# Performance work log

Measured on AMD Instinct MI355X. Metric: run time of the kernel, lower is better.

Reference implementation:

```python
import jax, jax.numpy as jnp
import numpy as np

VOCAB, EMBED, HIDDEN, LAYERS, CLASSES = 32000, 256, 256, 2, 2


def setup_inputs() -> dict:
    key = jax.random.key(0)
    ks = jax.random.split(key, 8)
    B, T = 64, 4096
    IN = EMBED + HIDDEN  # 512 (same for both layers since embed==hidden)
    tokens = jax.random.randint(ks[0], (B, T), 0, VOCAB)
    emb = jax.random.normal(ks[1], (VOCAB, EMBED), dtype=jnp.float32) * 0.05
    Wr = jax.random.normal(ks[2], (LAYERS, IN, HIDDEN), dtype=jnp.float32) * 0.05
    Wz = jax.random.normal(ks[3], (LAYERS, IN, HIDDEN), dtype=jnp.float32) * 0.05
    Wh = jax.random.normal(ks[4], (LAYERS, IN, HIDDEN), dtype=jnp.float32) * 0.05
    br = jnp.zeros((LAYERS, HIDDEN), dtype=jnp.float32)
    bz = jnp.full((LAYERS, HIDDEN), -2.0, dtype=jnp.float32)  # nn.init.constant_(bias_z, -2.0)
    bh = jnp.zeros((LAYERS, HIDDEN), dtype=jnp.float32)
    Wfc = jax.random.normal(ks[5], (HIDDEN, CLASSES), dtype=jnp.float32) * 0.05
    bfc = jnp.zeros((CLASSES,), dtype=jnp.float32)
    return dict(tokens=tokens, emb=emb, Wr=Wr, br=br, Wz=Wz, bz=bz, Wh=Wh, bh=bh, Wfc=Wfc, bfc=bfc)


def reference(tokens, emb, Wr, br, Wz, bz, Wh, bh, Wfc, bfc):
    B, T = tokens.shape
    x_seq = emb[tokens]                       # [B,T,E]
    xs = jnp.swapaxes(x_seq, 0, 1)            # [T,B,E] for scan over time
    h0 = jnp.zeros((LAYERS, B, HIDDEN), dtype=emb.dtype)

    def step(hs, xt):
        x = xt
        new_hs = []
        for i in range(LAYERS):
            h = hs[i]
            comb = jnp.concatenate([x, h], axis=1)          # [B, E+H]
            r = jax.nn.sigmoid(comb @ Wr[i] + br[i])
            z = jax.nn.sigmoid(comb @ Wz[i] + bz[i])
            comb_r = jnp.concatenate([x, r * h], axis=1)
            h_tilde = jnp.tanh(comb_r @ Wh[i] + bh[i])
            h = (1.0 - z) * h + z * h_tilde
            new_hs.append(h)
            x = h
        return jnp.stack(new_hs), None

    hs_final, _ = jax.lax.scan(step, h0, xs)
    # classification head on last timestep of last layer
    return hs_final[-1] @ Wfc + bfc             # [B, num_classes]
```

## Files before the change

### kernel.cpp

```cpp
#include <hip/hip_runtime.h>
#include <hip/hip_bf16.h>
#include <hip/hip_fp16.h>
#include <stdint.h>

typedef _Float16 h2_t  __attribute__((ext_vector_type(2)));
typedef _Float16 f16x8 __attribute__((ext_vector_type(8)));
typedef float    f32x4 __attribute__((ext_vector_type(4)));

#define TSEQ 4096
#define HID  256
#define IN2  512
#define NB   64
#define CH   256
#define NCH  16

__device__ __forceinline__ h2_t bc_h2(uint32_t v){ return __builtin_bit_cast(h2_t, v); }
__device__ __forceinline__ uint32_t pk2(float a, float b){
    h2_t p; p[0] = (_Float16)a; p[1] = (_Float16)b;
    return __builtin_bit_cast(uint32_t, p);
}

__device__ __forceinline__ float quad_reduce(float x){
    float t;
    t = __builtin_bit_cast(float, __builtin_amdgcn_mov_dpp(__builtin_bit_cast(int, x), 0xB1, 0xF, 0xF, true));
    x += t;
    t = __builtin_bit_cast(float, __builtin_amdgcn_mov_dpp(__builtin_bit_cast(int, x), 0x4E, 0xF, 0xF, true));
    x += t;
    return x;
}

__device__ __forceinline__ float sigm_(float x){
    return __builtin_amdgcn_rcpf(1.f + __expf(-x));
}
__device__ __forceinline__ float tanh_(float x){
    return 1.f - 2.f*__builtin_amdgcn_rcpf(1.f + __expf(2.f*x));
}

__device__ __forceinline__ void sync_lds(){
    asm volatile("s_waitcnt lgkmcnt(0)\n\ts_barrier" ::: "memory");
}

__global__ void prep_kernel(const float* __restrict__ Wr, const float* __restrict__ Wz,
                            const float* __restrict__ Wh, const float* __restrict__ emb,
                            const float* __restrict__ br, const float* __restrict__ bz,
                            const float* __restrict__ bh,
                            uint32_t* __restrict__ wpack, __half* __restrict__ wxt,
                            __half* __restrict__ embf16, float* __restrict__ biasv)
{
    const long long S0 = 2LL*3*128*256;
    const long long S1 = 2LL*768*256;
    const long long S2 = 32000LL*256;
    const long long S3 = 2LL*768;
    for (long long idx = (long long)blockIdx.x*256 + threadIdx.x; idx < S0+S1+S2+S3;
         idx += (long long)gridDim.x*256) {
        if (idx < S0) {
            int n   = (int)(idx & 255);
            int kk  = (int)((idx >> 8) & 127);
            int t   = (int)(idx >> 15);
            int g = t % 3, L = t / 3;
            const float* Wsrc = (g==0?Wr:(g==1?Wz:Wh)) + (size_t)L*IN2*HID;
            h2_t p;
            p[0] = (_Float16)Wsrc[(256 + kk)*HID + n];
            p[1] = (_Float16)Wsrc[(256 + 128 + kk)*HID + n];
            wpack[idx] = __builtin_bit_cast(uint32_t, p);
        } else if (idx < S0+S1) {
            int i  = (int)(idx - S0);
            int k  = i & 255;
            int i2 = i >> 8;
            int o  = i2 % 768, L = i2 / 768;
            int g  = o >> 8,   n = o & 255;
            const float* Wsrc = (g==0?Wr:(g==1?Wz:Wh)) + (size_t)L*IN2*HID;
            int ksrc = (L==1) ? ((k & 1) ? 128 + (k >> 1) : (k >> 1)) : k;
            wxt[i] = __float2half(Wsrc[ksrc*HID + n]);
        } else if (idx < S0+S1+S2) {
            int i = (int)(idx - S0 - S1);
            embf16[i] = __float2half(emb[i]);
        } else {
            int i = (int)(idx - S0 - S1 - S2);
            int o = i % 768, L = i / 768;
            int g = o >> 8,  n = o & 255;
            const float* bsrc = (g==0?br:(g==1?bz:bh));
            biasv[i] = bsrc[L*HID + n];
        }
    }
}

__global__ __launch_bounds__(256) void gemm_proj(
    const int* __restrict__ tokens, const __half* __restrict__ embf16,
    const __half* __restrict__ h0chunk, const __half* __restrict__ wxt,
    const float* __restrict__ biasv,
    __half* __restrict__ proj0, __half* __restrict__ proj1, int c0, int c1)
{
    const int Lz = blockIdx.z;
    const int c  = Lz ? c1 : c0;
    if (c < 0 || c >= NCH) return;
    __half* proj = Lz ? proj1 : proj0;

    __shared__ uint4 Ald[128*17];
    __shared__ uint4 Bld[64*17];
    const int tid = threadIdx.x;
    const int mt = blockIdx.x, nt = blockIdx.y;
    const int w = tid >> 6, l = tid & 63, lr = l & 15, lk = l >> 4;
    f32x4 acc[2][4] = {};

#pragma unroll 1
    for (int kh = 0; kh < 2; ++kh) {
        if (kh) __syncthreads();
#pragma unroll
        for (int it = 0; it < 8; ++it) {
            int idx = it*256 + tid;
            int row = idx >> 4, u4 = idx & 15;
            int grow = mt*128 + row;
            const __half* src;
            if (Lz == 0) {
                int b = grow >> 8, tl = grow & (CH-1);
                int tok = tokens[(size_t)b*TSEQ + c*CH + tl];
                src = embf16 + (size_t)tok*HID;
            } else {
                src = h0chunk + (size_t)grow*HID;
            }
            Ald[row*17 + u4] = ((const uint4*)(src + kh*128))[u4];
        }
#pragma unroll
        for (int it = 0; it < 4; ++it) {
            int idx = it*256 + tid;
            int col = idx >> 4, u4 = idx & 15;
            const __half* src = wxt + ((size_t)(Lz*768 + nt*64 + col))*HID + kh*128;
            Bld[col*17 + u4] = ((const uint4*)src)[u4];
        }
        __syncthreads();
        const _Float16* A = (const _Float16*)Ald;
        const _Float16* B = (const _Float16*)Bld;
#pragma unroll
        for (int kb = 0; kb < 4; ++kb) {
            int k0 = kb*32;
            f16x8 af[2], bf[4];
#pragma unroll
            for (int fm = 0; fm < 2; ++fm) {
                int row = w*32 + fm*16 + lr;
                af[fm] = *(const f16x8*)(A + row*136 + k0 + lk*8);
            }
#pragma unroll
            for (int fn = 0; fn < 4; ++fn) {
                int col = fn*16 + lr;
                bf[fn] = *(const f16x8*)(B + col*136 + k0 + lk*8);
            }
#pragma unroll
            for (int fm = 0; fm < 2; ++fm)
#pragma unroll
                for (int fn = 0; fn < 4; ++fn)
                    acc[fm][fn] = __builtin_amdgcn_mfma_f32_16x16x32_f16(af[fm], bf[fn], acc[fm][fn], 0,0,0);
        }
    }
#pragma unroll
    for (int fm = 0; fm < 2; ++fm)
#pragma unroll
        for (int fn = 0; fn < 4; ++fn)
#pragma unroll
            for (int q = 0; q < 4; ++q) {
                int row = mt*128 + w*32 + fm*16 + lk*4 + q;
                int col = nt*64 + fn*16 + lr;
                float v = acc[fm][fn][q] + biasv[Lz*768 + col];
                int nb2 = col & 127, g = col >> 8, hf2 = (col >> 7) & 1;
                proj[(size_t)row*1024 + nb2*8 + g*2 + hf2] = __float2half(v);
            }
}

__global__ __launch_bounds__(512)
__attribute__((amdgpu_waves_per_eu(2, 2)))
void rec_fused(
    const uint32_t* __restrict__ wpack,
    const __half* __restrict__ proj0, const __half* __restrict__ proj1,
    __half* __restrict__ h0chunk, float* __restrict__ hstate,
    const float* __restrict__ Wfc, const float* __restrict__ bfc,
    float* __restrict__ out, int c0, int c1)
{
    __shared__ __align__(16) uint32_t s_h[128];
    __shared__ __align__(16) uint32_t s_rh[128];
    __shared__ float s_head[256];

    const int L = blockIdx.x >> 6;
    const int b = blockIdx.x & 63;
    const int c = L ? c1 : c0;
    if (c < 0 || c >= NCH) return;

    const int tid = threadIdx.x;
    const int k4  = tid & 3;
    const int nb  = tid >> 2;
    const bool wlead = (k4 == 0);

    uint32_t wr_[2][32], wz_[2][32], wh_[2][32];
    {
        const uint32_t* wb = wpack + (size_t)(L*3*128)*256;
#pragma unroll
        for (int u = 0; u < 8; ++u)
#pragma unroll
            for (int j = 0; j < 4; ++j) {
                int i  = u*4 + j;
                int kk = k4*32 + (((u + k4) & 7)*4 + j);
                wr_[0][i] = wb[(      kk)*256 + nb      ];
                wr_[1][i] = wb[(      kk)*256 + nb + 128];
                wz_[0][i] = wb[(128 + kk)*256 + nb      ];
                wz_[1][i] = wb[(128 + kk)*256 + nb + 128];
                wh_[0][i] = wb[(256 + kk)*256 + nb      ];
                wh_[1][i] = wb[(256 + kk)*256 + nb + 128];
            }
    }
#pragma unroll
    for (int i = 0; i < 32; ++i) {
        asm volatile("" : "+v"(wr_[0][i]), "+v"(wr_[1][i]), "+v"(wz_[0][i]),
                          "+v"(wz_[1][i]), "+v"(wh_[0][i]), "+v"(wh_[1][i]));
    }

    float h0f, h1f;
    if (c == 0) { h0f = 0.f; h1f = 0.f; }
    else {
        h0f = hstate[(size_t)(L*NB + b)*HID + nb];
        h1f = hstate[(size_t)(L*NB + b)*HID + nb + 128];
    }
    if (wlead) s_h[nb] = pk2(h0f, h1f);
    __syncthreads();

    const uint4* prow = (const uint4*)((L ? proj1 : proj0) + (size_t)b*CH*1024);
    const uint4* hq4  = ((const uint4*)s_h)  + k4*8;
    const uint4* rq4  = ((const uint4*)s_rh) + k4*8;

    uint4 pj = prow[nb];

#pragma unroll 1
    for (int tl = 0; tl < CH; ++tl) {
        int tn = (tl + 1 < CH) ? tl + 1 : tl;
        uint4 pjN = prow[(size_t)tn*128 + nb];

        float ar0=0.f, ar1=0.f, az0=0.f, az1=0.f;
#pragma unroll
        for (int u = 0; u < 8; ++u) {
            uint4 hv = hq4[(u + k4) & 7];
            int i = u*4;
            ar0 = __builtin_amdgcn_fdot2(bc_h2(wr_[0][i  ]), bc_h2(hv.x), ar0, false);
            ar1 = __builtin_amdgcn_fdot2(bc_h2(wr_[1][i  ]), bc_h2(hv.x), ar1, false);
            az0 = __builtin_amdgcn_fdot2(bc_h2(wz_[0][i  ]), bc_h2(hv.x), az0, false);
            az1 = __builtin_amdgcn_fdot2(bc_h2(wz_[1][i  ]), bc_h2(hv.x), az1, false);
            ar0 = __builtin_amdgcn_fdot2(bc_h2(wr_[0][i+1]), bc_h2(hv.y), ar0, false);
            ar1 = __builtin_amdgcn_fdot2(bc_h2(wr_[1][i+1]), bc_h2(hv.y), ar1, false);
            az0 = __builtin_amdgcn_fdot2(bc_h2(wz_[0][i+1]), bc_h2(hv.y), az0, false);
            az1 = __builtin_amdgcn_fdot2(bc_h2(wz_[1][i+1]), bc_h2(hv.y), az1, false);
            ar0 = __builtin_amdgcn_fdot2(bc_h2(wr_[0][i+2]), bc_h2(hv.z), ar0, false);
            ar1 = __builtin_amdgcn_fdot2(bc_h2(wr_[1][i+2]), bc_h2(hv.z), ar1, false);
            az0 = __builtin_amdgcn_fdot2(bc_h2(wz_[0][i+2]), bc_h2(hv.z), az0, false);
            az1 = __builtin_amdgcn_fdot2(bc_h2(wz_[1][i+2]), bc_h2(hv.z), az1, false);
            ar0 = __builtin_amdgcn_fdot2(bc_h2(wr_[0][i+3]), bc_h2(hv.w), ar0, false);
            ar1 = __builtin_amdgcn_fdot2(bc_h2(wr_[1][i+3]), bc_h2(hv.w), ar1, false);
            az0 = __builtin_amdgcn_fdot2(bc_h2(wz_[0][i+3]), bc_h2(hv.w), az0, false);
            az1 = __builtin_amdgcn_fdot2(bc_h2(wz_[1][i+3]), bc_h2(hv.w), az1, false);
        }
        ar0 = quad_reduce(ar0); ar1 = quad_reduce(ar1);
        az0 = quad_reduce(az0); az1 = quad_reduce(az1);

        h2_t pjr = bc_h2(pj.x), pjz = bc_h2(pj.y);
        float r0 = sigm_(ar0 + (float)pjr[0]);
        float r1 = sigm_(ar1 + (float)pjr[1]);
        float z0 = sigm_(az0 + (float)pjz[0]);
        float z1 = sigm_(az1 + (float)pjz[1]);
        if (wlead) s_rh[nb] = pk2(r0*h0f, r1*h1f);
        sync_lds();

        float ah0a=0.f, ah0b=0.f, ah1a=0.f, ah1b=0.f;
#pragma unroll
        for (int u = 0; u < 8; ++u) {
            uint4 rv = rq4[(u + k4) & 7];
            int i = u*4;
            ah0a = __builtin_amdgcn_fdot2(bc_h2(wh_[0][i  ]), bc_h2(rv.x), ah0a, false);
            ah1a = __builtin_amdgcn_fdot2(bc_h2(wh_[1][i  ]), bc_h2(rv.x), ah1a, false);
            ah0b = __builtin_amdgcn_fdot2(bc_h2(wh_[0][i+1]), bc_h2(rv.y), ah0b, false);
            ah1b = __builtin_amdgcn_fdot2(bc_h2(wh_[1][i+1]), bc_h2(rv.y), ah1b, false);
            ah0a = __builtin_amdgcn_fdot2(bc_h2(wh_[0][i+2]), bc_h2(rv.z), ah0a, false);
            ah1a = __builtin_amdgcn_fdot2(bc_h2(wh_[1][i+2]), bc_h2(rv.z), ah1a, false);
            ah0b = __builtin_amdgcn_fdot2(bc_h2(wh_[0][i+3]), bc_h2(rv.w), ah0b, false);
            ah1b = __builtin_amdgcn_fdot2(bc_h2(wh_[1][i+3]), bc_h2(rv.w), ah1b, false);
        }
        float ah0 = quad_reduce(ah0a + ah0b);
        float ah1 = quad_reduce(ah1a + ah1b);

        h2_t pjh = bc_h2(pj.z);
        float t0 = tanh_(ah0 + (float)pjh[0]);
        float t1 = tanh_(ah1 + (float)pjh[1]);
        h0f += z0*(t0 - h0f);
        h1f += z1*(t1 - h1f);
        if (wlead) {
            uint32_t w2 = pk2(h0f, h1f);
            s_h[nb] = w2;
            if (L == 0)
                ((uint32_t*)h0chunk)[((size_t)b*CH + tl)*128 + nb] = w2;
        }
        pj = pjN;
        sync_lds();
    }

    if (wlead) {
        hstate[(size_t)(L*NB + b)*HID + nb]       = h0f;
        hstate[(size_t)(L*NB + b)*HID + nb + 128] = h1f;
    }

    if (L == 1 && c == NCH-1) {
        if (wlead) { s_head[nb] = h0f; s_head[nb+128] = h1f; }
        __syncthreads();
        if (tid < 64) {
            float p0 = 0.f, p1 = 0.f;
#pragma unroll
            for (int m = 0; m < 4; ++m) {
                float hv2 = s_head[tid + 64*m];
                p0 += hv2 * Wfc[(tid+64*m)*2+0];
                p1 += hv2 * Wfc[(tid+64*m)*2+1];
            }
#pragma unroll
            for (int d = 1; d < 64; d <<= 1) { p0 += __shfl_xor(p0, d); p1 += __shfl_xor(p1, d); }
            if (tid == 0) { out[b*2+0] = p0 + bfc[0]; out[b*2+1] = p1 + bfc[1]; }
        }
    }
}

extern "C" void kernel_launch(void* const* d_in, const int* in_sizes, int n_in,
                              void* d_out, int out_size, void* d_ws, size_t ws_size,
                              hipStream_t stream) {
    const int*   tokens = (const int*)  d_in[0];
    const float* emb    = (const float*)d_in[1];
    const float* Wr     = (const float*)d_in[2];
    const float* br     = (const float*)d_in[3];
    const float* Wz     = (const float*)d_in[4];
    const float* bz     = (const float*)d_in[5];
    const float* Wh     = (const float*)d_in[6];
    const float* bh     = (const float*)d_in[7];
    const float* Wfc    = (const float*)d_in[8];
    const float* bfc    = (const float*)d_in[9];
    float* out = (float*)d_out;

    char* ws = (char*)d_ws;
    uint32_t* wpack  = (uint32_t*)(ws + 0);
    __half*   wxt    = (__half*)(ws + (1u<<20));
    __half*   embf16 = (__half*)(ws + (2u<<20));
    __half*   proj0  = (__half*)(ws + 18874368u);
    __half*   proj1  = (__half*)(ws + 52428800u);
    __half*   h0chunk= (__half*)(ws + 85983232u);
    float*    hstate = (float*)(ws + 94371840u);
    float*    biasv  = (float*)(ws + 94502912u);

    prep_kernel<<<2048, 256, 0, stream>>>(Wr, Wz, Wh, emb, br, bz, bh, wpack, wxt, embf16, biasv);

    dim3 ggrid(128, 12, 2);
    for (int c = 0; c <= NCH; ++c) {
        int cc0 = (c < NCH) ? c : -1;
        int cc1 = c - 1;
        gemm_proj<<<ggrid, 256, 0, stream>>>(tokens, embf16, h0chunk, wxt, biasv, proj0, proj1, cc0, cc1);
        rec_fused<<<128, 512, 0, stream>>>(wpack, proj0, proj1, h0chunk, hstate, Wfc, bfc, out, cc0, cc1);
    }
}
```

Measured before the change: 7.011 ms.

## Fuse projection GEMM and recurrence into one launch with double-buffered pipelining

The separate projection GEMM and recurrence kernels are merged into a single launch per step. The first 128 blocks run the recurrence for chunk `step` (layer 0) and `step-2` (layer 1), while the remaining blocks compute projections for upcoming chunks into double-buffered proj and h0 buffers. This lets the small, latency-bound recurrence overlap with the GEMM instead of running serially. It also removes the fp16 embedding conversion pass by converting fp32 embeddings on the fly, compacts the proj layout to 768 halves per row, and uses 128x128 GEMM tiles. The cost is larger LDS per block, which may reduce occupancy for the recurrence blocks, and one extra pipeline step.

```diff
diff --git a/kernel.cpp b/kernel.cpp
--- a/kernel.cpp
+++ b/kernel.cpp
@@ -19,7 +19,6 @@
     h2_t p; p[0] = (_Float16)a; p[1] = (_Float16)b;
     return __builtin_bit_cast(uint32_t, p);
 }
-
 __device__ __forceinline__ float quad_reduce(float x){
     float t;
     t = __builtin_bit_cast(float, __builtin_amdgcn_mov_dpp(__builtin_bit_cast(int, x), 0xB1, 0xF, 0xF, true));
@@ -28,35 +27,34 @@
     x += t;
     return x;
 }
-
 __device__ __forceinline__ float sigm_(float x){
     return __builtin_amdgcn_rcpf(1.f + __expf(-x));
 }
 __device__ __forceinline__ float tanh_(float x){
     return 1.f - 2.f*__builtin_amdgcn_rcpf(1.f + __expf(2.f*x));
 }
-
 __device__ __forceinline__ void sync_lds(){
     asm volatile("s_waitcnt lgkmcnt(0)\n\ts_barrier" ::: "memory");
 }
+__device__ __forceinline__ f32x4 mfma16(f16x8 a, f16x8 b, f32x4 c){
+    return __builtin_amdgcn_mfma_f32_16x16x32_f16(a, b, c, 0, 0, 0);
+}
 
 __global__ void prep_kernel(const float* __restrict__ Wr, const float* __restrict__ Wz,
-                            const float* __restrict__ Wh, const float* __restrict__ emb,
+                            const float* __restrict__ Wh,
                             const float* __restrict__ br, const float* __restrict__ bz,
                             const float* __restrict__ bh,
                             uint32_t* __restrict__ wpack, __half* __restrict__ wxt,
-                            __half* __restrict__ embf16, float* __restrict__ biasv)
+                            float* __restrict__ biasv)
 {
-    const long long S0 = 2LL*3*128*256;
-    const long long S1 = 2LL*768*256;
-    const long long S2 = 32000LL*256;
-    const long long S3 = 2LL*768;
-    for (long long idx = (long long)blockIdx.x*256 + threadIdx.x; idx < S0+S1+S2+S3;
-         idx += (long long)gridDim.x*256) {
+    const int S0 = 196608;
+    const int S1 = 393216;
+    const int S3 = 1536;
+    for (int idx = blockIdx.x*256 + threadIdx.x; idx < S0+S1+S3; idx += gridDim.x*256) {
         if (idx < S0) {
-            int n   = (int)(idx & 255);
-            int kk  = (int)((idx >> 8) & 127);
-            int t   = (int)(idx >> 15);
+            int n  = idx & 255;
+            int kk = (idx >> 8) & 127;
+            int t  = idx >> 15;
             int g = t % 3, L = t / 3;
             const float* Wsrc = (g==0?Wr:(g==1?Wz:Wh)) + (size_t)L*IN2*HID;
             h2_t p;
@@ -64,19 +62,16 @@
             p[1] = (_Float16)Wsrc[(256 + 128 + kk)*HID + n];
             wpack[idx] = __builtin_bit_cast(uint32_t, p);
         } else if (idx < S0+S1) {
-            int i  = (int)(idx - S0);
+            int i  = idx - S0;
             int k  = i & 255;
             int i2 = i >> 8;
             int o  = i2 % 768, L = i2 / 768;
             int g  = o >> 8,   n = o & 255;
             const float* Wsrc = (g==0?Wr:(g==1?Wz:Wh)) + (size_t)L*IN2*HID;
             int ksrc = (L==1) ? ((k & 1) ? 128 + (k >> 1) : (k >> 1)) : k;
-            wxt[i] = __float2half(Wsrc[ksrc*HID + n]);
-        } else if (idx < S0+S1+S2) {
-            int i = (int)(idx - S0 - S1);
-            embf16[i] = __float2half(emb[i]);
+            wxt[i] = __float2half(Wsrc[(size_t)ksrc*HID + n]);
         } else {
-            int i = (int)(idx - S0 - S1 - S2);
+            int i = idx - S0 - S1;
             int o = i % 768, L = i / 768;
             int g = o >> 8,  n = o & 255;
             const float* bsrc = (g==0?br:(g==1?bz:bh));
@@ -85,238 +80,258 @@
     }
 }
 
-__global__ __launch_bounds__(256) void gemm_proj(
-    const int* __restrict__ tokens, const __half* __restrict__ embf16,
-    const __half* __restrict__ h0chunk, const __half* __restrict__ wxt,
-    const float* __restrict__ biasv,
-    __half* __restrict__ proj0, __half* __restrict__ proj1, int c0, int c1)
-{
-    const int Lz = blockIdx.z;
-    const int c  = Lz ? c1 : c0;
-    if (c < 0 || c >= NCH) return;
-    __half* proj = Lz ? proj1 : proj0;
-
-    __shared__ uint4 Ald[128*17];
-    __shared__ uint4 Bld[64*17];
-    const int tid = threadIdx.x;
-    const int mt = blockIdx.x, nt = blockIdx.y;
-    const int w = tid >> 6, l = tid & 63, lr = l & 15, lk = l >> 4;
-    f32x4 acc[2][4] = {};
-
-#pragma unroll 1
-    for (int kh = 0; kh < 2; ++kh) {
-        if (kh) __syncthreads();
-#pragma unroll
-        for (int it = 0; it < 8; ++it) {
-            int idx = it*256 + tid;
-            int row = idx >> 4, u4 = idx & 15;
-            int grow = mt*128 + row;
-            const __half* src;
-            if (Lz == 0) {
-                int b = grow >> 8, tl = grow & (CH-1);
-                int tok = tokens[(size_t)b*TSEQ + c*CH + tl];
-                src = embf16 + (size_t)tok*HID;
-            } else {
-                src = h0chunk + (size_t)grow*HID;
-            }
-            Ald[row*17 + u4] = ((const uint4*)(src + kh*128))[u4];
-        }
-#pragma unroll
-        for (int it = 0; it < 4; ++it) {
-            int idx = it*256 + tid;
-            int col = idx >> 4, u4 = idx & 15;
-            const __half* src = wxt + ((size_t)(Lz*768 + nt*64 + col))*HID + kh*128;
-            Bld[col*17 + u4] = ((const uint4*)src)[u4];
-        }
-        __syncthreads();
-        const _Float16* A = (const _Float16*)Ald;
-        const _Float16* B = (const _Float16*)Bld;
-#pragma unroll
-        for (int kb = 0; kb < 4; ++kb) {
-            int k0 = kb*32;
-            f16x8 af[2], bf[4];
-#pragma unroll
-            for (int fm = 0; fm < 2; ++fm) {
-                int row = w*32 + fm*16 + lr;
-                af[fm] = *(const f16x8*)(A + row*136 + k0 + lk*8);
-            }
-#pragma unroll
-            for (int fn = 0; fn < 4; ++fn) {
-                int col = fn*16 + lr;
-                bf[fn] = *(const f16x8*)(B + col*136 + k0 + lk*8);
-            }
-#pragma unroll
-            for (int fm = 0; fm < 2; ++fm)
-#pragma unroll
-                for (int fn = 0; fn < 4; ++fn)
-                    acc[fm][fn] = __builtin_amdgcn_mfma_f32_16x16x32_f16(af[fm], bf[fn], acc[fm][fn], 0,0,0);
-        }
-    }
-#pragma unroll
-    for (int fm = 0; fm < 2; ++fm)
-#pragma unroll
-        for (int fn = 0; fn < 4; ++fn)
-#pragma unroll
-            for (int q = 0; q < 4; ++q) {
-                int row = mt*128 + w*32 + fm*16 + lk*4 + q;
-                int col = nt*64 + fn*16 + lr;
-                float v = acc[fm][fn][q] + biasv[Lz*768 + col];
-                int nb2 = col & 127, g = col >> 8, hf2 = (col >> 7) & 1;
-                proj[(size_t)row*1024 + nb2*8 + g*2 + hf2] = __float2half(v);
-            }
-}
-
 __global__ __launch_bounds__(512)
 __attribute__((amdgpu_waves_per_eu(2, 2)))
-void rec_fused(
-    const uint32_t* __restrict__ wpack,
-    const __half* __restrict__ proj0, const __half* __restrict__ proj1,
-    __half* __restrict__ h0chunk, float* __restrict__ hstate,
-    const float* __restrict__ Wfc, const float* __restrict__ bfc,
-    float* __restrict__ out, int c0, int c1)
+void fused_step(const int* __restrict__ tokens, const float* __restrict__ emb,
+                const uint32_t* __restrict__ wpack, const __half* __restrict__ wxt,
+                const float* __restrict__ biasv,
+                __half* __restrict__ proj0a, __half* __restrict__ proj0b,
+                __half* __restrict__ proj1a, __half* __restrict__ proj1b,
+                __half* __restrict__ h0a, __half* __restrict__ h0b,
+                float* __restrict__ hstate,
+                const float* __restrict__ Wfc, const float* __restrict__ bfc,
+                float* __restrict__ out, int step)
 {
     __shared__ __align__(16) uint32_t s_h[128];
     __shared__ __align__(16) uint32_t s_rh[128];
     __shared__ float s_head[256];
-
-    const int L = blockIdx.x >> 6;
-    const int b = blockIdx.x & 63;
-    const int c = L ? c1 : c0;
-    if (c < 0 || c >= NCH) return;
+    __shared__ uint4 Ald[128*17];
+    __shared__ uint4 Bld[128*17];
 
     const int tid = threadIdx.x;
-    const int k4  = tid & 3;
-    const int nb  = tid >> 2;
-    const bool wlead = (k4 == 0);
-
-    uint32_t wr_[2][32], wz_[2][32], wh_[2][32];
-    {
-        const uint32_t* wb = wpack + (size_t)(L*3*128)*256;
-#pragma unroll
-        for (int u = 0; u < 8; ++u)
-#pragma unroll
-            for (int j = 0; j < 4; ++j) {
-                int i  = u*4 + j;
-                int kk = k4*32 + (((u + k4) & 7)*4 + j);
-                wr_[0][i] = wb[(      kk)*256 + nb      ];
-                wr_[1][i] = wb[(      kk)*256 + nb + 128];
-                wz_[0][i] = wb[(128 + kk)*256 + nb      ];
-                wz_[1][i] = wb[(128 + kk)*256 + nb + 128];
-                wh_[0][i] = wb[(256 + kk)*256 + nb      ];
-                wh_[1][i] = wb[(256 + kk)*256 + nb + 128];
-            }
-    }
-#pragma unroll
-    for (int i = 0; i < 32; ++i) {
-        asm volatile("" : "+v"(wr_[0][i]), "+v"(wr_[1][i]), "+v"(wz_[0][i]),
-                          "+v"(wz_[1][i]), "+v"(wh_[0][i]), "+v"(wh_[1][i]));
-    }
-
-    float h0f, h1f;
-    if (c == 0) { h0f = 0.f; h1f = 0.f; }
-    else {
-        h0f = hstate[(size_t)(L*NB + b)*HID + nb];
-        h1f = hstate[(size_t)(L*NB + b)*HID + nb + 128];
-    }
-    if (wlead) s_h[nb] = pk2(h0f, h1f);
-    __syncthreads();
-
-    const uint4* prow = (const uint4*)((L ? proj1 : proj0) + (size_t)b*CH*1024);
-    const uint4* hq4  = ((const uint4*)s_h)  + k4*8;
-    const uint4* rq4  = ((const uint4*)s_rh) + k4*8;
-
-    uint4 pj = prow[nb];
+
+    if (blockIdx.x < 128) {
+        const int L = blockIdx.x >> 6;
+        const int b = blockIdx.x & 63;
+        const int c = L ? (step - 2) : step;
+        if (c < 0 || c >= NCH) return;
+        const uint32_t* projr = (const uint32_t*)(L ? ((step & 1) ? proj1b : proj1a)
+                                                    : ((step & 1) ? proj0b : proj0a));
+        uint32_t* h0w = (uint32_t*)((step & 1) ? h0b : h0a);
+
+        const int k4  = tid & 3;
+        const int nb  = tid >> 2;
+        const bool wlead = (k4 == 0);
+
+        uint32_t wr_[2][32], wz_[2][32], wh_[2][32];
+        {
+            const uint32_t* wb = wpack + (size_t)(L*3*128)*256;
+#pragma unroll
+            for (int u = 0; u < 8; ++u)
+#pragma unroll
+                for (int j = 0; j < 4; ++j) {
+                    int i  = u*4 + j;
+                    int kk = k4*32 + (((u + k4) & 7)*4 + j);
+                    wr_[0][i] = wb[(      kk)*256 + nb      ];
+                    wr_[1][i] = wb[(      kk)*256 + nb + 128];
+                    wz_[0][i] = wb[(128 + kk)*256 + nb      ];
+                    wz_[1][i] = wb[(128 + kk)*256 + nb + 128];
+                    wh_[0][i] = wb[(256 + kk)*256 + nb      ];
+                    wh_[1][i] = wb[(256 + kk)*256 + nb + 128];
+                }
+        }
+#pragma unroll
+        for (int i = 0; i < 32; ++i) {
+            asm volatile("" : "+v"(wr_[0][i]), "+v"(wr_[1][i]), "+v"(wz_[0][i]),
+                              "+v"(wz_[1][i]), "+v"(wh_[0][i]), "+v"(wh_[1][i]));
+        }
+
+        float h0f, h1f;
+        if (c == 0) { h0f = 0.f; h1f = 0.f; }
+        else {
+            h0f = hstate[(size_t)(L*NB + b)*HID + nb];
+            h1f = hstate[(size_t)(L*NB + b)*HID + nb + 128];
+        }
+        if (wlead) s_h[nb] = pk2(h0f, h1f);
+        __syncthreads();
+
+        const uint32_t* prow = projr + (size_t)b*CH*384;
+        const uint4* hq4  = ((const uint4*)s_h)  + k4*8;
+        const uint4* rq4  = ((const uint4*)s_rh) + k4*8;
+
+        uint2    pjrz = *(const uint2*)(prow + nb*2);
+        uint32_t pjh  = prow[256 + nb];
 
 #pragma unroll 1
-    for (int tl = 0; tl < CH; ++tl) {
-        int tn = (tl + 1 < CH) ? tl + 1 : tl;
-        uint4 pjN = prow[(size_t)tn*128 + nb];
-
-        float ar0=0.f, ar1=0.f, az0=0.f, az1=0.f;
-#pragma unroll
-        for (int u = 0; u < 8; ++u) {
-            uint4 hv = hq4[(u + k4) & 7];
-            int i = u*4;
-            ar0 = __builtin_amdgcn_fdot2(bc_h2(wr_[0][i  ]), bc_h2(hv.x), ar0, false);
-            ar1 = __builtin_amdgcn_fdot2(bc_h2(wr_[1][i  ]), bc_h2(hv.x), ar1, false);
-            az0 = __builtin_amdgcn_fdot2(bc_h2(wz_[0][i  ]), bc_h2(hv.x), az0, false);
-            az1 = __builtin_amdgcn_fdot2(bc_h2(wz_[1][i  ]), bc_h2(hv.x), az1, false);
-            ar0 = __builtin_amdgcn_fdot2(bc_h2(wr_[0][i+1]), bc_h2(hv.y), ar0, false);
-            ar1 = __builtin_amdgcn_fdot2(bc_h2(wr_[1][i+1]), bc_h2(hv.y), ar1, false);
-            az0 = __builtin_amdgcn_fdot2(bc_h2(wz_[0][i+1]), bc_h2(hv.y), az0, false);
-            az1 = __builtin_amdgcn_fdot2(bc_h2(wz_[1][i+1]), bc_h2(hv.y), az1, false);
-            ar0 = __builtin_amdgcn_fdot2(bc_h2(wr_[0][i+2]), bc_h2(hv.z), ar0, false);
-            ar1 = __builtin_amdgcn_fdot2(bc_h2(wr_[1][i+2]), bc_h2(hv.z), ar1, false);
-            az0 = __builtin_amdgcn_fdot2(bc_h2(wz_[0][i+2]), bc_h2(hv.z), az0, false);
-            az1 = __builtin_amdgcn_fdot2(bc_h2(wz_[1][i+2]), bc_h2(hv.z), az1, false);
-            ar0 = __builtin_amdgcn_fdot2(bc_h2(wr_[0][i+3]), bc_h2(hv.w), ar0, false);
-            ar1 = __builtin_amdgcn_fdot2(bc_h2(wr_[1][i+3]), bc_h2(hv.w), ar1, false);
-            az0 = __builtin_amdgcn_fdot2(bc_h2(wz_[0][i+3]), bc_h2(hv.w), az0, false);
-            az1 = __builtin_amdgcn_fdot2(bc_h2(wz_[1][i+3]), bc_h2(hv.w), az1, false);
-        }
-        ar0 = quad_reduce(ar0); ar1 = quad_reduce(ar1);
-        az0 = quad_reduce(az0); az1 = quad_reduce(az1);
-
-        h2_t pjr = bc_h2(pj.x), pjz = bc_h2(pj.y);
-        float r0 = sigm_(ar0 + (float)pjr[0]);
-        float r1 = sigm_(ar1 + (float)pjr[1]);
-        float z0 = sigm_(az0 + (float)pjz[0]);
-        float z1 = sigm_(az1 + (float)pjz[1]);
-        if (wlead) s_rh[nb] = pk2(r0*h0f, r1*h1f);
-        sync_lds();
-
-        float ah0a=0.f, ah0b=0.f, ah1a=0.f, ah1b=0.f;
-#pragma unroll
-        for (int u = 0; u < 8; ++u) {
-            uint4 rv = rq4[(u + k4) & 7];
-            int i = u*4;
-            ah0a = __builtin_amdgcn_fdot2(bc_h2(wh_[0][i  ]), bc_h2(rv.x), ah0a, false);
-            ah1a = __builtin_amdgcn_fdot2(bc_h2(wh_[1][i  ]), bc_h2(rv.x), ah1a, false);
-            ah0b = __builtin_amdgcn_fdot2(bc_h2(wh_[0][i+1]), bc_h2(rv.y), ah0b, false);
-            ah1b = __builtin_amdgcn_fdot2(bc_h2(wh_[1][i+1]), bc_h2(rv.y), ah1b, false);
-            ah0a = __builtin_amdgcn_fdot2(bc_h2(wh_[0][i+2]), bc_h2(rv.z), ah0a, false);
-            ah1a = __builtin_amdgcn_fdot2(bc_h2(wh_[1][i+2]), bc_h2(rv.z), ah1a, false);
-            ah0b = __builtin_amdgcn_fdot2(bc_h2(wh_[0][i+3]), bc_h2(rv.w), ah0b, false);
-            ah1b = __builtin_amdgcn_fdot2(bc_h2(wh_[1][i+3]), bc_h2(rv.w), ah1b, false);
-        }
-        float ah0 = quad_reduce(ah0a + ah0b);
-        float ah1 = quad_reduce(ah1a + ah1b);
-
-        h2_t pjh = bc_h2(pj.z);
-        float t0 = tanh_(ah0 + (float)pjh[0]);
-        float t1 = tanh_(ah1 + (float)pjh[1]);
-        h0f += z0*(t0 - h0f);
-        h1f += z1*(t1 - h1f);
+        for (int tl = 0; tl < CH; ++tl) {
+            int tn = (tl + 1 < CH) ? tl + 1 : tl;
+            const uint32_t* pn = prow + (size_t)tn*384;
+            uint2    pjrzN = *(const uint2*)(pn + nb*2);
+            uint32_t pjhN  = pn[256 + nb];
+
+            float ar0=0.f, ar1=0.f, az0=0.f, az1=0.f;
+#pragma unroll
+            for (int u = 0; u < 8; ++u) {
+                uint4 hv = hq4[(u + k4) & 7];
+                int i = u*4;
+                ar0 = __builtin_amdgcn_fdot2(bc_h2(wr_[0][i  ]), bc_h2(hv.x), ar0, false);
+                ar1 = __builtin_amdgcn_fdot2(bc_h2(wr_[1][i  ]), bc_h2(hv.x), ar1, false);
+                az0 = __builtin_amdgcn_fdot2(bc_h2(wz_[0][i  ]), bc_h2(hv.x), az0, false);
+                az1 = __builtin_amdgcn_fdot2(bc_h2(wz_[1][i  ]), bc_h2(hv.x), az1, false);
+                ar0 = __builtin_amdgcn_fdot2(bc_h2(wr_[0][i+1]), bc_h2(hv.y), ar0, false);
+                ar1 = __builtin_amdgcn_fdot2(bc_h2(wr_[1][i+1]), bc_h2(hv.y), ar1, false);
+                az0 = __builtin_amdgcn_fdot2(bc_h2(wz_[0][i+1]), bc_h2(hv.y), az0, false);
+                az1 = __builtin_amdgcn_fdot2(bc_h2(wz_[1][i+1]), bc_h2(hv.y), az1, false);
+                ar0 = __builtin_amdgcn_fdot2(bc_h2(wr_[0][i+2]), bc_h2(hv.z), ar0, false);
+                ar1 = __builtin_amdgcn_fdot2(bc_h2(wr_[1][i+2]), bc_h2(hv.z), ar1, false);
+                az0 = __builtin_amdgcn_fdot2(bc_h2(wz_[0][i+2]), bc_h2(hv.z), az0, false);
+                az1 = __builtin_amdgcn_fdot2(bc_h2(wz_[1][i+2]), bc_h2(hv.z), az1, false);
+                ar0 = __builtin_amdgcn_fdot2(bc_h2(wr_[0][i+3]), bc_h2(hv.w), ar0, false);
+                ar1 = __builtin_amdgcn_fdot2(bc_h2(wr_[1][i+3]), bc_h2(hv.w), ar1, false);
+                az0 = __builtin_amdgcn_fdot2(bc_h2(wz_[0][i+3]), bc_h2(hv.w), az0, false);
+                az1 = __builtin_amdgcn_fdot2(bc_h2(wz_[1][i+3]), bc_h2(hv.w), az1, false);
+            }
+            ar0 = quad_reduce(ar0); ar1 = quad_reduce(ar1);
+            az0 = quad_reduce(az0); az1 = quad_reduce(az1);
+
+            h2_t pjr = bc_h2(pjrz.x), pjz = bc_h2(pjrz.y);
+            float r0 = sigm_(ar0 + (float)pjr[0]);
+            float r1 = sigm_(ar1 + (float)pjr[1]);
+            float z0 = sigm_(az0 + (float)pjz[0]);
+            float z1 = sigm_(az1 + (float)pjz[1]);
+            if (wlead) s_rh[nb] = pk2(r0*h0f, r1*h1f);
+            sync_lds();
+
+            float ah0a=0.f, ah0b=0.f, ah1a=0.f, ah1b=0.f;
+#pragma unroll
+            for (int u = 0; u < 8; ++u) {
+                uint4 rv = rq4[(u + k4) & 7];
+                int i = u*4;
+                ah0a = __builtin_amdgcn_fdot2(bc_h2(wh_[0][i  ]), bc_h2(rv.x), ah0a, false);
+                ah1a = __builtin_amdgcn_fdot2(bc_h2(wh_[1][i  ]), bc_h2(rv.x), ah1a, false);
+                ah0b = __builtin_amdgcn_fdot2(bc_h2(wh_[0][i+1]), bc_h2(rv.y), ah0b, false);
+                ah1b = __builtin_amdgcn_fdot2(bc_h2(wh_[1][i+1]), bc_h2(rv.y), ah1b, false);
+                ah0a = __builtin_amdgcn_fdot2(bc_h2(wh_[0][i+2]), bc_h2(rv.z), ah0a, false);
+                ah1a = __builtin_amdgcn_fdot2(bc_h2(wh_[1][i+2]), bc_h2(rv.z), ah1a, false);
+                ah0b = __builtin_amdgcn_fdot2(bc_h2(wh_[0][i+3]), bc_h2(rv.w), ah0b, false);
+                ah1b = __builtin_amdgcn_fdot2(bc_h2(wh_[1][i+3]), bc_h2(rv.w), ah1b, false);
+            }
+            float ah0 = quad_reduce(ah0a + ah0b);
+            float ah1 = quad_reduce(ah1a + ah1b);
+
+            h2_t pjh2 = bc_h2(pjh);
+            float t0 = tanh_(ah0 + (float)pjh2[0]);
+            float t1 = tanh_(ah1 + (float)pjh2[1]);
+            h0f += z0*(t0 - h0f);
+            h1f += z1*(t1 - h1f);
+            if (wlead) {
+                uint32_t w2 = pk2(h0f, h1f);
+                s_h[nb] = w2;
+                if (L == 0)
+                    h0w[((size_t)b*CH + tl)*128 + nb] = w2;
+            }
+            pjrz = pjrzN; pjh = pjhN;
+            sync_lds();
+        }
+
         if (wlead) {
-            uint32_t w2 = pk2(h0f, h1f);
-            s_h[nb] = w2;
-            if (L == 0)
-                ((uint32_t*)h0chunk)[((size_t)b*CH + tl)*128 + nb] = w2;
-        }
-        pj = pjN;
-        sync_lds();
-    }
-
-    if (wlead) {
-        hstate[(size_t)(L*NB + b)*HID + nb]       = h0f;
-        hstate[(size_t)(L*NB + b)*HID + nb + 128] = h1f;
-    }
-
-    if (L == 1 && c == NCH-1) {
-        if (wlead) { s_head[nb] = h0f; s_head[nb+128] = h1f; }
-        __syncthreads();
-        if (tid < 64) {
-            float p0 = 0.f, p1 = 0.f;
-#pragma unroll
-            for (int m = 0; m < 4; ++m) {
-                float hv2 = s_head[tid + 64*m];
-                p0 += hv2 * Wfc[(tid+64*m)*2+0];
-                p1 += hv2 * Wfc[(tid+64*m)*2+1];
-            }
-#pragma unroll
-            for (int d = 1; d < 64; d <<= 1) { p0 += __shfl_xor(p0, d); p1 += __shfl_xor(p1, d); }
-            if (tid == 0) { out[b*2+0] = p0 + bfc[0]; out[b*2+1] = p1 + bfc[1]; }
-        }
+            hstate[(size_t)(L*NB + b)*HID + nb]       = h0f;
+            hstate[(size_t)(L*NB + b)*HID + nb + 128] = h1f;
+        }
+
+        if (L == 1 && c == NCH-1) {
+            if (wlead) { s_head[nb] = h0f; s_head[nb+128] = h1f; }
+            __syncthreads();
+            if (tid < 64) {
+                float p0 = 0.f, p1 = 0.f;
+#pragma unroll
+                for (int m = 0; m < 4; ++m) {
+                    float hv2 = s_head[tid + 64*m];
+                    p0 += hv2 * Wfc[(tid+64*m)*2+0];
+                    p1 += hv2 * Wfc[(tid+64*m)*2+1];
+                }
+#pragma unroll
+                for (int d = 1; d < 64; d <<= 1) { p0 += __shfl_xor(p0, d); p1 += __shfl_xor(p1, d); }
+                if (tid == 0) { out[b*2+0] = p0 + bfc[0]; out[b*2+1] = p1 + bfc[1]; }
+            }
+        }
+    } else {
+        int gb = blockIdx.x - 128;
+        const int Lz = (gb >= 768) ? 1 : 0;
+        gb -= Lz * 768;
+        const int mt = gb / 6, nt = gb % 6;
+        const int c = Lz ? (step - 1) : (step + 1);
+        if (c < 0 || c >= NCH) return;
+        __half* projw = Lz ? (((step + 1) & 1) ? proj1b : proj1a)
+                           : (((step + 1) & 1) ? proj0b : proj0a);
+        const __half* h0r = ((step - 1) & 1) ? h0b : h0a;
+
+        const int w  = tid >> 6;
+        const int wm = w >> 2, wn = w & 3;
+        const int l  = tid & 63, lr = l & 15, lk = l >> 4;
+        f32x4 acc[4][2] = {};
+
+#pragma unroll 1
+        for (int kh = 0; kh < 2; ++kh) {
+            if (kh) __syncthreads();
+            if (Lz == 0) {
+#pragma unroll
+                for (int it = 0; it < 4; ++it) {
+                    int idx = it*512 + tid;
+                    int row = idx >> 4, seg = idx & 15;
+                    int grow = mt*128 + row;
+                    int bb = grow >> 8, tl = grow & 255;
+                    int tok = tokens[(size_t)bb*TSEQ + c*CH + tl];
+                    const float* s = emb + (size_t)tok*HID + kh*128 + seg*8;
+                    float4 f0 = *(const float4*)s;
+                    float4 f1 = *(const float4*)(s + 4);
+                    uint4 v;
+                    v.x = __builtin_bit_cast(uint32_t, __builtin_amdgcn_cvt_pkrtz(f0.x, f0.y));
+                    v.y = __builtin_bit_cast(uint32_t, __builtin_amdgcn_cvt_pkrtz(f0.z, f0.w));
+                    v.z = __builtin_bit_cast(uint32_t, __builtin_amdgcn_cvt_pkrtz(f1.x, f1.y));
+                    v.w = __builtin_bit_cast(uint32_t, __builtin_amdgcn_cvt_pkrtz(f1.z, f1.w));
+                    Ald[row*17 + seg] = v;
+                }
+            } else {
+#pragma unroll
+                for (int it = 0; it < 4; ++it) {
+                    int idx = it*512 + tid;
+                    int row = idx >> 4, u4 = idx & 15;
+                    int grow = mt*128 + row;
+                    const __half* src = h0r + (size_t)grow*HID + kh*128;
+                    Ald[row*17 + u4] = ((const uint4*)src)[u4];
+                }
+            }
+#pragma unroll
+            for (int it = 0; it < 4; ++it) {
+                int idx = it*512 + tid;
+                int col = idx >> 4, u4 = idx & 15;
+                const __half* src = wxt + ((size_t)(Lz*768 + nt*128 + col))*HID + kh*128;
+                Bld[col*17 + u4] = ((const uint4*)src)[u4];
+            }
+            __syncthreads();
+            const _Float16* A = (const _Float16*)Ald;
+            const _Float16* B = (const _Float16*)Bld;
+#pragma unroll
+            for (int kb = 0; kb < 4; ++kb) {
+                int k0 = kb*32;
+                f16x8 af[4], bf[2];
+#pragma unroll
+                for (int fm = 0; fm < 4; ++fm)
+                    af[fm] = *(const f16x8*)(A + (wm*64 + fm*16 + lr)*136 + k0 + lk*8);
+#pragma unroll
+                for (int fn = 0; fn < 2; ++fn)
+                    bf[fn] = *(const f16x8*)(B + (wn*32 + fn*16 + lr)*136 + k0 + lk*8);
+#pragma unroll
+                for (int fm = 0; fm < 4; ++fm)
+#pragma unroll
+                    for (int fn = 0; fn < 2; ++fn)
+                        acc[fm][fn] = mfma16(af[fm], bf[fn], acc[fm][fn]);
+            }
+        }
+#pragma unroll
+        for (int fm = 0; fm < 4; ++fm)
+#pragma unroll
+            for (int fn = 0; fn < 2; ++fn)
+#pragma unroll
+                for (int q = 0; q < 4; ++q) {
+                    int row = mt*128 + wm*64 + fm*16 + lk*4 + q;
+                    int col = nt*128 + wn*32 + fn*16 + lr;
+                    float v = acc[fm][fn][q] + biasv[Lz*768 + col];
+                    int nb2 = col & 127, g = col >> 8, hf = (col >> 7) & 1;
+                    int fidx = (g == 2) ? (512 + nb2*2 + hf) : (nb2*4 + g*2 + hf);
+                    projw[(size_t)row*768 + fidx] = __float2half(v);
+                }
     }
 }
 
@@ -337,21 +352,21 @@
 
     char* ws = (char*)d_ws;
     uint32_t* wpack  = (uint32_t*)(ws + 0);
-    __half*   wxt    = (__half*)(ws + (1u<<20));
-    __half*   embf16 = (__half*)(ws + (2u<<20));
-    __half*   proj0  = (__half*)(ws + 18874368u);
-    __half*   proj1  = (__half*)(ws + 52428800u);
-    __half*   h0chunk= (__half*)(ws + 85983232u);
-    float*    hstate = (float*)(ws + 94371840u);
-    float*    biasv  = (float*)(ws + 94502912u);
-
-    prep_kernel<<<2048, 256, 0, stream>>>(Wr, Wz, Wh, emb, br, bz, bh, wpack, wxt, embf16, biasv);
-
-    dim3 ggrid(128, 12, 2);
-    for (int c = 0; c <= NCH; ++c) {
-        int cc0 = (c < NCH) ? c : -1;
-        int cc1 = c - 1;
-        gemm_proj<<<ggrid, 256, 0, stream>>>(tokens, embf16, h0chunk, wxt, biasv, proj0, proj1, cc0, cc1);
-        rec_fused<<<128, 512, 0, stream>>>(wpack, proj0, proj1, h0chunk, hstate, Wfc, bfc, out, cc0, cc1);
+    __half*   wxt    = (__half*)(ws +    786432u);
+    __half*   proj0a = (__half*)(ws +   1572864u);
+    __half*   proj0b = (__half*)(ws +  26738688u);
+    __half*   proj1a = (__half*)(ws +  51904512u);
+    __half*   proj1b = (__half*)(ws +  77070336u);
+    __half*   h0a    = (__half*)(ws + 102236160u);
+    __half*   h0b    = (__half*)(ws + 110624768u);
+    float*    hstate = (float*)(ws + 119013376u);
+    float*    biasv  = (float*)(ws + 119144448u);
+
+    prep_kernel<<<1024, 256, 0, stream>>>(Wr, Wz, Wh, br, bz, bh, wpack, wxt, biasv);
+
+    for (int i = -1; i <= 17; ++i) {
+        fused_step<<<1664, 512, 0, stream>>>(tokens, emb, wpack, wxt, biasv,
+                                             proj0a, proj0b, proj1a, proj1b,
+                                             h0a, h0b, hstate, Wfc, bfc, out, i);
     }
 }
```

New measurement: 5.919 ms. -15.6%, faster.
